# Optimization experiments

Measured on AMD Instinct MI355X. Metric: run time of the kernel, lower is better.

Reference implementation:

```python
import jax, jax.numpy as jnp
import numpy as np

ITERATIONS = 3

def setup_inputs() -> dict:
    key = jax.random.key(0)
    k1, k2 = jax.random.split(key)
    C, S, H = 64, 128, 2048
    x = jax.random.normal(k1, (C, S, H), dtype=jnp.float32)
    W = jax.random.normal(k2, (H, H), dtype=jnp.float32)
    return {"x": x, "W": W}

def reference(x, W):
    # x: [C, S, H], W: [H, H]
    C, S, H = x.shape
    # e_ij is loop-invariant in the original; hoist it (same math, computed once)
    e_ij = jnp.einsum('csh,hk->csk', x, W)  # [C, S, H]
    b_ij = jnp.zeros((C, S), dtype=x.dtype)
    c_i = jnp.zeros((C, H), dtype=x.dtype)
    for _ in range(ITERATIONS):
        d_i = jax.nn.softmax(b_ij, axis=1)[:, :, None]          # [C, S, 1], softmax over S
        c_i = jnp.sum(d_i * e_ij, axis=1)                        # [C, H]
        squared = jnp.sum(c_i ** 2, axis=1, keepdims=True)       # [C, 1]
        coeff = squared / (1.0 + squared) / jnp.sqrt(squared + 1e-9)
        c_i = coeff * c_i                                        # squash
        b_ij = b_ij + jnp.einsum('csh,ch->cs', e_ij, c_i)        # logit update
    return c_i
```

## Files before the change

kernel.cpp:

```cpp
#include <hip/hip_runtime.h>

using bf16x8 = __attribute__((ext_vector_type(8))) __bf16;
using f32x4  = __attribute__((ext_vector_type(4))) float;

#define C_ 64
#define S_ 128
#define H_ 2048
#define M_ 8192

__device__ __forceinline__ unsigned short f2bf(float f) {
  unsigned u = __float_as_uint(f);
  u = u + 0x7fffu + ((u >> 16) & 1u);
  return (unsigned short)(u >> 16);
}
__device__ __forceinline__ float bf2f(unsigned short h) {
  return __uint_as_float(((unsigned)h) << 16);
}

__device__ __forceinline__ void glds16(const unsigned short* g, unsigned short* l) {
  __builtin_amdgcn_global_load_lds(
      (const __attribute__((address_space(1))) void*)g,
      (__attribute__((address_space(3))) void*)l, 16, 0, 0);
}

__global__ void k_split_all(const float* __restrict__ x,
                            unsigned short* __restrict__ xh,
                            unsigned short* __restrict__ xl,
                            const float* __restrict__ W,
                            unsigned short* __restrict__ Wth,
                            unsigned short* __restrict__ Wtl,
                            float* __restrict__ G) {
  __shared__ float Ts[64][68];
  const int b = blockIdx.x;
  const int t = threadIdx.x;
  if (b < 16384) {
    int idx = b * 256 + t;
    float4 v = ((const float4*)x)[idx];
    float a[4] = {v.x, v.y, v.z, v.w};
    unsigned short h[4], l[4];
#pragma unroll
    for (int q = 0; q < 4; ++q) {
      h[q] = f2bf(a[q]);
      l[q] = f2bf(a[q] - bf2f(h[q]));
    }
    ((ushort4*)xh)[idx] = make_ushort4(h[0], h[1], h[2], h[3]);
    ((ushort4*)xl)[idx] = make_ushort4(l[0], l[1], l[2], l[3]);
  } else if (b < 17408) {
    const int bb = b - 16384;
    const int k0 = (bb & 31) * 64, n0 = (bb >> 5) * 64;
#pragma unroll
    for (int p = 0; p < 4; ++p) {
      int idx = t + p * 256;
      int r = idx >> 4, c4 = (idx & 15) * 4;
      *(float4*)&Ts[r][c4] = *(const float4*)(W + (size_t)(k0 + r) * H_ + n0 + c4);
    }
    __syncthreads();
#pragma unroll
    for (int p = 0; p < 4; ++p) {
      int idx = t + p * 256;
      int rr = idx >> 4, cc = (idx & 15) * 4;
      unsigned short h[4], l[4];
#pragma unroll
      for (int q = 0; q < 4; ++q) {
        float f = Ts[cc + q][rr];
        h[q] = f2bf(f);
        l[q] = f2bf(f - bf2f(h[q]));
      }
      size_t o = (size_t)(n0 + rr) * H_ + k0 + cc;
      *(ushort4*)(Wth + o) = make_ushort4(h[0], h[1], h[2], h[3]);
      *(ushort4*)(Wtl + o) = make_ushort4(l[0], l[1], l[2], l[3]);
    }
  } else {
    const int bb = b - 17408;
    ((float4*)G)[bb * 256 + t] = (float4){0.f, 0.f, 0.f, 0.f};
  }
}

#define TILE_USH 24576
#define OFF_AH 0
#define OFF_AL 8192
#define OFF_BH 16384
#define OFF_BL 20480

#define LOADSET(AH, AL, BH, BL, off)                                  \
  do {                                                                \
    const int _o = (off);                                             \
    _Pragma("unroll") for (int i = 0; i < 4; ++i) {                   \
      AH[i] = *(const bf16x8*)&lds[_o + OFF_AH + rA + i * 512];       \
      AL[i] = *(const bf16x8*)&lds[_o + OFF_AL + rA + i * 512];       \
      BH[i] = *(const bf16x8*)&lds[_o + OFF_BH + rB + i * 512];       \
      BL[i] = *(const bf16x8*)&lds[_o + OFF_BL + rB + i * 512];       \
    }                                                                 \
  } while (0)

#define MFMASET(AH, AL, BH, BL)                                                                  \
  do {                                                                                           \
    __builtin_amdgcn_s_setprio(1);                                                               \
    _Pragma("unroll") for (int i = 0; i < 4; ++i)                                                \
        _Pragma("unroll") for (int j = 0; j < 4; ++j) {                                          \
      acc[i][j] = __builtin_amdgcn_mfma_f32_16x16x32_bf16(AH[i], BH[j], acc[i][j], 0, 0, 0);     \
      acc[i][j] = __builtin_amdgcn_mfma_f32_16x16x32_bf16(AH[i], BL[j], acc[i][j], 0, 0, 0);     \
      acc[i][j] = __builtin_amdgcn_mfma_f32_16x16x32_bf16(AL[i], BH[j], acc[i][j], 0, 0, 0);     \
    }                                                                                            \
    __builtin_amdgcn_s_setprio(0);                                                               \
  } while (0)

__global__ __launch_bounds__(512, 2) void k_gemm3(
    const unsigned short* __restrict__ Ah, const unsigned short* __restrict__ Al,
    const unsigned short* __restrict__ Bh, const unsigned short* __restrict__ Bl,
    unsigned short* __restrict__ Eh, unsigned short* __restrict__ El) {
  __shared__ unsigned short lds[3 * TILE_USH];
  const int t = threadIdx.x;
  const int lane = t & 63, wid = t >> 6;
  const int wm = wid >> 1, wn = wid & 1;
  const int l16 = lane & 15, quad = lane >> 4;

  const int lin = blockIdx.x + (blockIdx.y << 5);
  const int xcd = lin & 7, slot = lin >> 3;
  const int bm = ((xcd >> 1) << 3) + (slot >> 3);
  const int bn = ((xcd & 1) << 3) + (slot & 7);

  const int rl = lane >> 2;
  const int gg8 = (((lane & 3) ^ ((rl >> 1) & 3)) << 3);
  const unsigned short* gAh0 = Ah + (size_t)(bm * 256 + wid * 16 + rl) * H_ + gg8;
  const unsigned short* gAl0 = Al + (size_t)(bm * 256 + wid * 16 + rl) * H_ + gg8;
  const unsigned short* gAh1 = gAh0 + (size_t)128 * H_;
  const unsigned short* gAl1 = gAl0 + (size_t)128 * H_;
  const unsigned short* gBh  = Bh + (size_t)(bn * 128 + wid * 16 + rl) * H_ + gg8;
  const unsigned short* gBl  = Bl + (size_t)(bn * 128 + wid * 16 + rl) * H_ + gg8;
  const int dA0 = wid * 512;
  const int dA1 = dA0 + 4096;
  const int dB  = wid * 512;

  const int colq = ((quad ^ ((l16 >> 1) & 3)) << 3);
  const int rA = (wm * 64 + l16) * 32 + colq;
  const int rB = (wn * 64 + l16) * 32 + colq;

  f32x4 acc[4][4];
#pragma unroll
  for (int i = 0; i < 4; ++i)
#pragma unroll
    for (int j = 0; j < 4; ++j) acc[i][j] = (f32x4)0.f;

  auto stage6 = [&](int bo, int k) {
    glds16(gAh0 + k, &lds[bo + OFF_AH + dA0]);
    glds16(gAh1 + k, &lds[bo + OFF_AH + dA1]);
    glds16(gAl0 + k, &lds[bo + OFF_AL + dA0]);
    glds16(gAl1 + k, &lds[bo + OFF_AL + dA1]);
    glds16(gBh + k,  &lds[bo + OFF_BH + dB]);
    glds16(gBl + k,  &lds[bo + OFF_BL + dB]);
  };

  stage6(0, 0);
  stage6(TILE_USH, 32);
  asm volatile("s_waitcnt vmcnt(6)" ::: "memory");
  __builtin_amdgcn_s_barrier();
  __builtin_amdgcn_sched_barrier(0);

  bf16x8 ahA[4], alA[4], bhA[4], blA[4];
  bf16x8 ahB[4], alB[4], bhB[4], blB[4];
  LOADSET(ahA, alA, bhA, blA, 0);

  int stage_off = 2 * TILE_USH;
  int read_off  = TILE_USH;

#pragma unroll 1
  for (int tt = 0; tt < 62; tt += 2) {
    stage6(stage_off, (tt + 2) * 32);
    stage_off += TILE_USH; if (stage_off == 3 * TILE_USH) stage_off = 0;
    asm volatile("s_waitcnt vmcnt(6) lgkmcnt(0)" ::: "memory");
    __builtin_amdgcn_s_barrier();
    __builtin_amdgcn_sched_barrier(0);
    LOADSET(ahB, alB, bhB, blB, read_off);
    read_off += TILE_USH; if (read_off == 3 * TILE_USH) read_off = 0;
    __builtin_amdgcn_sched_barrier(0);
    MFMASET(ahA, alA, bhA, blA);
    stage6(stage_off, (tt + 3) * 32);
    stage_off += TILE_USH; if (stage_off == 3 * TILE_USH) stage_off = 0;
    asm volatile("s_waitcnt vmcnt(6) lgkmcnt(0)" ::: "memory");
    __builtin_amdgcn_s_barrier();
    __builtin_amdgcn_sched_barrier(0);
    LOADSET(ahA, alA, bhA, blA, read_off);
    read_off += TILE_USH; if (read_off == 3 * TILE_USH) read_off = 0;
    __builtin_amdgcn_sched_barrier(0);
    MFMASET(ahB, alB, bhB, blB);
  }

  asm volatile("s_waitcnt vmcnt(0) lgkmcnt(0)" ::: "memory");
  __builtin_amdgcn_s_barrier();
  __builtin_amdgcn_sched_barrier(0);
  LOADSET(ahB, alB, bhB, blB, read_off);
  __builtin_amdgcn_sched_barrier(0);
  MFMASET(ahA, alA, bhA, blA);
  MFMASET(ahB, alB, bhB, blB);

#pragma unroll
  for (int i = 0; i < 4; ++i) {
    const int row0 = bm * 256 + wm * 64 + i * 16 + quad * 4;
#pragma unroll
    for (int j = 0; j < 4; ++j) {
      const int col = bn * 128 + wn * 64 + j * 16 + l16;
#pragma unroll
      for (int r = 0; r < 4; ++r) {
        float v = acc[i][j][r];
        unsigned short hh = f2bf(v);
        unsigned short ll = f2bf(v - bf2f(hh));
        Eh[(size_t)(row0 + r) * H_ + col] = hh;
        El[(size_t)(row0 + r) * H_ + col] = ll;
      }
    }
  }
}

__global__ __launch_bounds__(256, 4) void k_gram_mfma(
    const unsigned short* __restrict__ Eh, const unsigned short* __restrict__ El,
    float* __restrict__ G) {
  __shared__ unsigned short sH[128 * 32], sL[128 * 32];
  const int t = threadIdx.x;
  const int kc = blockIdx.x;
  const int cc = blockIdx.y;
  const int lane = t & 63, wid = t >> 6;
  const int wm = wid >> 1, wn = wid & 1;
  const int l16 = lane & 15, quad = lane >> 4;

  const int rl = lane >> 2;
  const int gg = (lane & 3) ^ ((rl >> 1) & 3);
  const int c0 = wid * 2, c1 = c0 + 1;
  const unsigned short* gH0 = Eh + (size_t)(cc * 128 + c0 * 16 + rl) * H_ + gg * 8;
  const unsigned short* gH1 = Eh + (size_t)(cc * 128 + c1 * 16 + rl) * H_ + gg * 8;
  const unsigned short* gL0 = El + (size_t)(cc * 128 + c0 * 16 + rl) * H_ + gg * 8;
  const unsigned short* gL1 = El + (size_t)(cc * 128 + c1 * 16 + rl) * H_ + gg * 8;
  unsigned short* lH0 = sH + c0 * 512;
  unsigned short* lH1 = sH + c1 * 512;
  unsigned short* lL0 = sL + c0 * 512;
  unsigned short* lL1 = sL + c1 * 512;

  const int swz = ((l16 >> 1) & 3);
  const int colq = ((quad ^ swz) * 8);

  f32x4 acc[4][4];
#pragma unroll
  for (int i = 0; i < 4; ++i)
#pragma unroll
    for (int j = 0; j < 4; ++j) acc[i][j] = (f32x4)0.f;

  const int kbeg = kc * 512;
  for (int k0 = kbeg; k0 < kbeg + 512; k0 += 32) {
    __syncthreads();
    glds16(gH0 + k0, lH0);
    glds16(gH1 + k0, lH1);
    glds16(gL0 + k0, lL0);
    glds16(gL1 + k0, lL1);
    __syncthreads();

    bf16x8 ah[4], al[4], bh[4], bl[4];
#pragma unroll
    for (int i = 0; i < 4; ++i) {
      const int ra = (wm * 64 + i * 16 + l16) * 32;
      const int rb = (wn * 64 + i * 16 + l16) * 32;
      ah[i] = *(const bf16x8*)&sH[ra + colq];
      al[i] = *(const bf16x8*)&sL[ra + colq];
      bh[i] = *(const bf16x8*)&sH[rb + colq];
      bl[i] = *(const bf16x8*)&sL[rb + colq];
    }
#pragma unroll
    for (int i = 0; i < 4; ++i)
#pragma unroll
      for (int j = 0; j < 4; ++j) {
        acc[i][j] = __builtin_amdgcn_mfma_f32_16x16x32_bf16(ah[i], bh[j], acc[i][j], 0, 0, 0);
        acc[i][j] = __builtin_amdgcn_mfma_f32_16x16x32_bf16(ah[i], bl[j], acc[i][j], 0, 0, 0);
        acc[i][j] = __builtin_amdgcn_mfma_f32_16x16x32_bf16(al[i], bh[j], acc[i][j], 0, 0, 0);
      }
  }

  float* Gc = G + (size_t)cc * S_ * S_;
#pragma unroll
  for (int i = 0; i < 4; ++i) {
    const int row0 = wm * 64 + i * 16 + quad * 4;
#pragma unroll
    for (int j = 0; j < 4; ++j) {
      const int col = wn * 64 + j * 16 + l16;
#pragma unroll
      for (int r = 0; r < 4; ++r)
        atomicAdd(&Gc[(row0 + r) * S_ + col], acc[i][j][r]);
    }
  }
}

__global__ void k_out2(const unsigned short* __restrict__ Eh,
                       const unsigned short* __restrict__ El,
                       const float* __restrict__ G, float* __restrict__ out) {
  const int c = blockIdx.y;
  const int s = threadIdx.x & 127;
  __shared__ float dsh[128];
  __shared__ float red[128];
  __shared__ float wsh[128];
  const float* Gc = G + (size_t)c * S_ * S_;
  float b = 0.f;
  for (int it = 0; it < 3; ++it) {
    red[s] = b; __syncthreads();
    for (int off = 64; off > 0; off >>= 1) {
      if (s < off) red[s] = fmaxf(red[s], red[s + off]);
      __syncthreads();
    }
    float mx = red[0]; __syncthreads();
    float ev = expf(b - mx);
    red[s] = ev; __syncthreads();
    for (int off = 64; off > 0; off >>= 1) {
      if (s < off) red[s] = red[s] + red[s + off];
      __syncthreads();
    }
    float Z = red[0]; __syncthreads();
    float d = ev / Z;
    dsh[s] = d; __syncthreads();
    float y = 0.f;
#pragma unroll 8
    for (int j = 0; j < S_; ++j) y = fmaf(Gc[j * S_ + s], dsh[j], y);
    red[s] = d * y; __syncthreads();
    for (int off = 64; off > 0; off >>= 1) {
      if (s < off) red[s] = red[s] + red[s + off];
      __syncthreads();
    }
    float sq = red[0]; __syncthreads();
    float coeff = sq / (1.f + sq) / sqrtf(sq + 1e-9f);
    if (it == 2) wsh[s] = coeff * d;
    else b += coeff * y;
  }
  __syncthreads();

  const int h2 = blockIdx.x * 256 + threadIdx.x;
  const unsigned* Ph = (const unsigned*)(Eh + (size_t)c * S_ * H_) + h2;
  const unsigned* Pl = (const unsigned*)(El + (size_t)c * S_ * H_) + h2;
  float a0 = 0.f, a1 = 0.f;
#pragma unroll 8
  for (int ss = 0; ss < S_; ++ss) {
    unsigned uh = Ph[(size_t)ss * (H_ / 2)];
    unsigned ul = Pl[(size_t)ss * (H_ / 2)];
    a0 = fmaf(wsh[ss], bf2f((unsigned short)uh) + bf2f((unsigned short)ul), a0);
    a1 = fmaf(wsh[ss], bf2f((unsigned short)(uh >> 16)) + bf2f((unsigned short)(ul >> 16)), a1);
  }
  ((float2*)(out + (size_t)c * H_))[h2] = make_float2(a0, a1);
}

extern "C" void kernel_launch(void* const* d_in, const int* in_sizes, int n_in,
                              void* d_out, int out_size, void* d_ws, size_t ws_size,
                              hipStream_t stream) {
  (void)in_sizes; (void)n_in; (void)out_size; (void)ws_size;
  const float* x = (const float*)d_in[0];
  const float* W = (const float*)d_in[1];
  float* out = (float*)d_out;
  char* ws = (char*)d_ws;

  unsigned short* xh  = (unsigned short*)(ws);
  unsigned short* xl  = (unsigned short*)(ws + 33554432);
  unsigned short* Wth = (unsigned short*)(ws + 67108864);
  unsigned short* Wtl = (unsigned short*)(ws + 75497472);
  unsigned short* Eh  = (unsigned short*)(ws + 83886080);
  unsigned short* El  = (unsigned short*)(ws + 117440512);
  float*          G   = (float*)(ws + 150994944);

  k_split_all<<<dim3(18432), 256, 0, stream>>>(x, xh, xl, W, Wth, Wtl, G);
  k_gemm3<<<dim3(32, 16), 512, 0, stream>>>(xh, xl, Wth, Wtl, Eh, El);
  k_gram_mfma<<<dim3(4, 64), 256, 0, stream>>>(Eh, El, G);
  k_out2<<<dim3(4, 64), 256, 0, stream>>>(Eh, El, G, out);
}
```

Before: 338.1 us.

## Double-buffer gram kernel loads and use inline-asm LDS reads in GEMM

```diff
diff --git a/kernel.cpp b/kernel.cpp
--- a/kernel.cpp
+++ b/kernel.cpp
@@ -82,15 +82,21 @@
 #define OFF_BH 16384
 #define OFF_BL 20480
 
-#define LOADSET(AH, AL, BH, BL, off)                                  \
-  do {                                                                \
-    const int _o = (off);                                             \
-    _Pragma("unroll") for (int i = 0; i < 4; ++i) {                   \
-      AH[i] = *(const bf16x8*)&lds[_o + OFF_AH + rA + i * 512];       \
-      AL[i] = *(const bf16x8*)&lds[_o + OFF_AL + rA + i * 512];       \
-      BH[i] = *(const bf16x8*)&lds[_o + OFF_BH + rB + i * 512];       \
-      BL[i] = *(const bf16x8*)&lds[_o + OFF_BL + rB + i * 512];       \
-    }                                                                 \
+#define DSREAD(dst, addr, OFFLIT) \
+  asm volatile("ds_read_b128 %0, %1 offset:" OFFLIT : "=v"(dst) : "v"(addr))
+
+#define LOADSET_ASM(AH, AL, BH, BL, off_ush)                      \
+  do {                                                            \
+    unsigned _ab = aAb + (unsigned)(off_ush) * 2u;                \
+    unsigned _bb = aBb + (unsigned)(off_ush) * 2u;                \
+    DSREAD(AH[0], _ab, "0");     DSREAD(AH[1], _ab, "1024");      \
+    DSREAD(AH[2], _ab, "2048");  DSREAD(AH[3], _ab, "3072");      \
+    DSREAD(AL[0], _ab, "16384"); DSREAD(AL[1], _ab, "17408");     \
+    DSREAD(AL[2], _ab, "18432"); DSREAD(AL[3], _ab, "19456");     \
+    DSREAD(BH[0], _bb, "32768"); DSREAD(BH[1], _bb, "33792");     \
+    DSREAD(BH[2], _bb, "34816"); DSREAD(BH[3], _bb, "35840");     \
+    DSREAD(BL[0], _bb, "40960"); DSREAD(BL[1], _bb, "41984");     \
+    DSREAD(BL[2], _bb, "43008"); DSREAD(BL[3], _bb, "44032");     \
   } while (0)
 
 #define MFMASET(AH, AL, BH, BL)                                                                  \
@@ -135,6 +141,9 @@
   const int colq = ((quad ^ ((l16 >> 1) & 3)) << 3);
   const int rA = (wm * 64 + l16) * 32 + colq;
   const int rB = (wn * 64 + l16) * 32 + colq;
+  const unsigned ldsb = (unsigned)(uintptr_t)&lds[0];
+  const unsigned aAb = ldsb + (unsigned)rA * 2u;
+  const unsigned aBb = ldsb + (unsigned)rB * 2u;
 
   f32x4 acc[4][4];
 #pragma unroll
@@ -159,7 +168,7 @@
 
   bf16x8 ahA[4], alA[4], bhA[4], blA[4];
   bf16x8 ahB[4], alB[4], bhB[4], blB[4];
-  LOADSET(ahA, alA, bhA, blA, 0);
+  LOADSET_ASM(ahA, alA, bhA, blA, 0);
 
   int stage_off = 2 * TILE_USH;
   int read_off  = TILE_USH;
@@ -171,7 +180,7 @@
     asm volatile("s_waitcnt vmcnt(6) lgkmcnt(0)" ::: "memory");
     __builtin_amdgcn_s_barrier();
     __builtin_amdgcn_sched_barrier(0);
-    LOADSET(ahB, alB, bhB, blB, read_off);
+    LOADSET_ASM(ahB, alB, bhB, blB, read_off);
     read_off += TILE_USH; if (read_off == 3 * TILE_USH) read_off = 0;
     __builtin_amdgcn_sched_barrier(0);
     MFMASET(ahA, alA, bhA, blA);
@@ -180,7 +189,7 @@
     asm volatile("s_waitcnt vmcnt(6) lgkmcnt(0)" ::: "memory");
     __builtin_amdgcn_s_barrier();
     __builtin_amdgcn_sched_barrier(0);
-    LOADSET(ahA, alA, bhA, blA, read_off);
+    LOADSET_ASM(ahA, alA, bhA, blA, read_off);
     read_off += TILE_USH; if (read_off == 3 * TILE_USH) read_off = 0;
     __builtin_amdgcn_sched_barrier(0);
     MFMASET(ahB, alB, bhB, blB);
@@ -189,9 +198,11 @@
   asm volatile("s_waitcnt vmcnt(0) lgkmcnt(0)" ::: "memory");
   __builtin_amdgcn_s_barrier();
   __builtin_amdgcn_sched_barrier(0);
-  LOADSET(ahB, alB, bhB, blB, read_off);
+  LOADSET_ASM(ahB, alB, bhB, blB, read_off);
   __builtin_amdgcn_sched_barrier(0);
   MFMASET(ahA, alA, bhA, blA);
+  asm volatile("s_waitcnt lgkmcnt(0)" ::: "memory");
+  __builtin_amdgcn_sched_barrier(0);
   MFMASET(ahB, alB, bhB, blB);
 
 #pragma unroll
@@ -215,7 +226,7 @@
 __global__ __launch_bounds__(256, 4) void k_gram_mfma(
     const unsigned short* __restrict__ Eh, const unsigned short* __restrict__ El,
     float* __restrict__ G) {
-  __shared__ unsigned short sH[128 * 32], sL[128 * 32];
+  __shared__ unsigned short sb[2][16384];
   const int t = threadIdx.x;
   const int kc = blockIdx.x;
   const int cc = blockIdx.y;
@@ -230,10 +241,7 @@
   const unsigned short* gH1 = Eh + (size_t)(cc * 128 + c1 * 16 + rl) * H_ + gg * 8;
   const unsigned short* gL0 = El + (size_t)(cc * 128 + c0 * 16 + rl) * H_ + gg * 8;
   const unsigned short* gL1 = El + (size_t)(cc * 128 + c1 * 16 + rl) * H_ + gg * 8;
-  unsigned short* lH0 = sH + c0 * 512;
-  unsigned short* lH1 = sH + c1 * 512;
-  unsigned short* lL0 = sL + c0 * 512;
-  unsigned short* lL1 = sL + c1 * 512;
+  const int dH0 = c0 * 512, dH1 = c1 * 512;
 
   const int swz = ((l16 >> 1) & 3);
   const int colq = ((quad ^ swz) * 8);
@@ -244,15 +252,24 @@
 #pragma unroll
     for (int j = 0; j < 4; ++j) acc[i][j] = (f32x4)0.f;
 
+  auto stage4 = [&](int buf, int k) {
+    glds16(gH0 + k, &sb[buf][dH0]);
+    glds16(gH1 + k, &sb[buf][dH1]);
+    glds16(gL0 + k, &sb[buf][8192 + dH0]);
+    glds16(gL1 + k, &sb[buf][8192 + dH1]);
+  };
+
   const int kbeg = kc * 512;
-  for (int k0 = kbeg; k0 < kbeg + 512; k0 += 32) {
-    __syncthreads();
-    glds16(gH0 + k0, lH0);
-    glds16(gH1 + k0, lH1);
-    glds16(gL0 + k0, lL0);
-    glds16(gL1 + k0, lL1);
-    __syncthreads();
-
+  stage4(0, kbeg);
+  asm volatile("s_waitcnt vmcnt(0)" ::: "memory");
+  __builtin_amdgcn_s_barrier();
+
+  int cur = 0;
+#pragma unroll 1
+  for (int s = 0; s < 16; ++s) {
+    if (s < 15) stage4(cur ^ 1, kbeg + (s + 1) * 32);
+    const unsigned short* sH = &sb[cur][0];
+    const unsigned short* sL = &sb[cur][8192];
     bf16x8 ah[4], al[4], bh[4], bl[4];
 #pragma unroll
     for (int i = 0; i < 4; ++i) {
@@ -263,6 +280,7 @@
       bh[i] = *(const bf16x8*)&sH[rb + colq];
       bl[i] = *(const bf16x8*)&sL[rb + colq];
     }
+    __builtin_amdgcn_s_setprio(1);
 #pragma unroll
     for (int i = 0; i < 4; ++i)
 #pragma unroll
@@ -271,6 +289,12 @@
         acc[i][j] = __builtin_amdgcn_mfma_f32_16x16x32_bf16(ah[i], bl[j], acc[i][j], 0, 0, 0);
         acc[i][j] = __builtin_amdgcn_mfma_f32_16x16x32_bf16(al[i], bh[j], acc[i][j], 0, 0, 0);
       }
+    __builtin_amdgcn_s_setprio(0);
+    if (s < 15) {
+      asm volatile("s_waitcnt vmcnt(0) lgkmcnt(0)" ::: "memory");
+      __builtin_amdgcn_s_barrier();
+    }
+    cur ^= 1;
   }
 
   float* Gc = G + (size_t)cc * S_ * S_;
```

Result: no change. 333.1 us (-1.5%).
